# Performance work log

Hardware: AMD Instinct MI355X
Metric: run time of the kernel (lower is better)

## Reference

```python
import jax, jax.numpy as jnp
import numpy as np

D_MODEL = 1024
NHEAD = 16
D_HEAD = D_MODEL // NHEAD


def setup_inputs() -> dict:
    key = jax.random.key(0)
    ks = jax.random.split(key, 5)
    s_in = 1.0 / np.sqrt(D_MODEL)
    x = jax.random.normal(ks[0], (2, 2048, D_MODEL), dtype=jnp.float32)
    Wqkv = jax.random.uniform(ks[1], (D_MODEL, 3 * D_MODEL), jnp.float32, -s_in, s_in)
    bqkv = jax.random.uniform(ks[2], (3 * D_MODEL,), jnp.float32, -s_in, s_in)
    Wproj = jax.random.uniform(ks[3], (D_MODEL, D_MODEL), jnp.float32, -s_in, s_in)
    bproj = jax.random.uniform(ks[4], (D_MODEL,), jnp.float32, -s_in, s_in)
    return {"x": x, "Wqkv": Wqkv, "bqkv": bqkv, "Wproj": Wproj, "bproj": bproj}


def reference(x, Wqkv, bqkv, Wproj, bproj):
    B, N, D = x.shape
    qkv = x @ Wqkv + bqkv                       # [B, N, 3D]
    q, k, v = jnp.split(qkv, 3, axis=-1)
    # [B, N, D] -> [B, H, N, d]
    def to_heads(t):
        return t.reshape(B, N, NHEAD, D_HEAD).transpose(0, 2, 1, 3)
    q, k, v = to_heads(q), to_heads(k), to_heads(v)
    scale = 1.0 / np.sqrt(D_HEAD).astype(np.float32)
    attn = jnp.einsum('bhqd,bhkd->bhqk', q, k) * scale
    attn = jax.nn.softmax(attn, axis=-1)
    y = jnp.einsum('bhqk,bhkd->bhqd', attn, v)  # [B, H, N, d]
    y = y.transpose(0, 2, 1, 3).reshape(B, N, D)
    return y @ Wproj + bproj
```

## Files before the change

### kernel.cpp

```cpp
#include <hip/hip_runtime.h>
#include <hip/hip_bf16.h>
#include <stdint.h>

typedef __hip_bfloat16 bf16;
typedef __attribute__((ext_vector_type(8))) short short8;
typedef __attribute__((ext_vector_type(4))) float f32x4;

#define QSCALE 0.18033688011f

__device__ __forceinline__ float fast_exp2(float x) {
#if __has_builtin(__builtin_amdgcn_exp2f)
  return __builtin_amdgcn_exp2f(x);
#else
  return exp2f(x);
#endif
}

__device__ __forceinline__ uint32_t pack2_bf16(float a, float b) {
#if __has_builtin(__builtin_amdgcn_cvt_pk_bf16_f32)
  typedef __attribute__((ext_vector_type(2))) __bf16 bf16x2;
  bf16x2 v = __builtin_amdgcn_cvt_pk_bf16_f32(a, b);
  return __builtin_bit_cast(uint32_t, v);
#else
  uint32_t ua = __builtin_bit_cast(uint32_t, a);
  uint32_t ub = __builtin_bit_cast(uint32_t, b);
  ua += 0x7FFF + ((ua >> 16) & 1);
  ub += 0x7FFF + ((ub >> 16) & 1);
  return (ua >> 16) | (ub & 0xFFFF0000u);
#endif
}

__device__ __forceinline__ void gload_lds16(const bf16* g, bf16* l) {
#if __has_builtin(__builtin_amdgcn_global_load_lds)
  __builtin_amdgcn_global_load_lds(
      (const __attribute__((address_space(1))) void*)(uintptr_t)g,
      (__attribute__((address_space(3))) void*)(uint32_t)(uintptr_t)l,
      16, 0, 0);
#else
  int lane = threadIdx.x & 63;
  *(short8*)(l + lane * 8) = *(const short8*)(g + lane * 8);
#endif
}

#define VM4_BARRIER() \
  asm volatile("s_waitcnt vmcnt(4)\n\ts_barrier" ::: "memory")
#define VM3_BARRIER() \
  asm volatile("s_waitcnt vmcnt(3)\n\ts_barrier" ::: "memory")
#define LDSR_BARRIER() \
  asm volatile("s_waitcnt lgkmcnt(0)\n\ts_barrier" ::: "memory")
#define DMA_BARRIER() \
  asm volatile("s_waitcnt vmcnt(0) lgkmcnt(0)\n\ts_barrier" ::: "memory")

__device__ __forceinline__ void transpose_tile(const float* __restrict__ in,
                                               bf16* __restrict__ out,
                                               int R, int C, int bx, int by,
                                               bf16 (*t)[72]) {
  const int r0 = by * 64, c0 = bx * 64;
  const int rr = threadIdx.x >> 3, cc = (threadIdx.x & 7) * 8;
#pragma unroll
  for (int rep = 0; rep < 2; ++rep) {
    int y = rr + rep * 32;
    const float* p = in + (size_t)(r0 + y) * C + c0 + cc;
    f32x4 v0 = *(const f32x4*)p;
    f32x4 v1 = *(const f32x4*)(p + 4);
#pragma unroll
    for (int j = 0; j < 4; ++j) {
      t[cc + j][y] = __float2bfloat16(v0[j]);
      t[cc + 4 + j][y] = __float2bfloat16(v1[j]);
    }
  }
  __syncthreads();
#pragma unroll
  for (int rep = 0; rep < 2; ++rep) {
    int y = rr + rep * 32;
    short8 v = *(const short8*)&t[y][cc];
    *(short8*)(out + (size_t)(c0 + y) * R + r0 + cc) = v;
  }
}

__global__ __launch_bounds__(256)
void prep_k(const float* __restrict__ x, bf16* __restrict__ xb,
            const float* __restrict__ Wqkv, bf16* __restrict__ WtQkv,
            const float* __restrict__ Wproj, bf16* __restrict__ WtP) {
  __shared__ __align__(16) bf16 t[64][72];
  const int bid = blockIdx.x;
  if (bid < 2048) {
    int i = (bid * 256 + threadIdx.x) * 8;
    f32x4 v0 = *(const f32x4*)(x + i);
    f32x4 v1 = *(const f32x4*)(x + i + 4);
    short8 r;
    bf16* rb = (bf16*)&r;
#pragma unroll
    for (int j = 0; j < 4; ++j) {
      rb[j] = __float2bfloat16(v0[j]);
      rb[4 + j] = __float2bfloat16(v1[j]);
    }
    *(short8*)(xb + i) = r;
  } else if (bid < 2048 + 768) {
    int b = bid - 2048;
    transpose_tile(Wqkv, WtQkv, 1024, 3072, b % 48, b / 48, t);
  } else {
    int b = bid - 2816;
    transpose_tile(Wproj, WtP, 1024, 1024, b % 16, b / 16, t);
  }
}

template <int MODE, int TM>
__global__ __launch_bounds__(256, (TM == 128) ? 3 : 2)
void gemm_bt(const bf16* __restrict__ A, const bf16* __restrict__ Bt,
             const float* __restrict__ bias, float* __restrict__ outp,
             bf16* __restrict__ Qd, bf16* __restrict__ Kd, bf16* __restrict__ Vt,
             int M, int Nn, int K) {
  constexpr int MI = TM / 32;
  constexpr int BUFE = TM * 32 + 4096;
  __shared__ __align__(16) bf16 smem[2 * BUFE];

  const int tid = threadIdx.x;
  const int wave = tid >> 6, lane = tid & 63;
  const int quad = lane >> 4, l16 = lane & 15;
  const int mw = (wave >> 1) * (TM / 2), nw = (wave & 1) * 64;

  const int nwg = gridDim.x * gridDim.y;
  const int ord = blockIdx.y * gridDim.x + blockIdx.x;
  const int wg = (ord & 7) * (nwg >> 3) + (ord >> 3);
  const int m_blk = (wg / gridDim.x) * TM, n_blk = (wg % gridDim.x) * 128;

  f32x4 acc[MI][4];
#pragma unroll
  for (int i = 0; i < MI; ++i)
#pragma unroll
    for (int j = 0; j < 4; ++j) acc[i][j] = (f32x4){0.f, 0.f, 0.f, 0.f};

  const int rowA = lane >> 2, colA = (lane & 3) * 8;
  const int chunkB = wave * 2;
  const bf16* gB = Bt + (size_t)(n_blk + chunkB * 16 + rowA) * K + colA;
  const int chunkA = (TM == 128) ? wave * 2 : wave;
  const bf16* gA = A + (size_t)(m_blk + chunkA * 16 + rowA) * K + colA;

  const int oA0 = chunkA * 512;
  const int oA1 = (chunkA + 1) * 512;
  const int oB0 = TM * 32 + chunkB * 512;
  const int oB1 = TM * 32 + (chunkB + 1) * 512;

  gload_lds16(gA, smem + oA0);
  if (TM == 128) gload_lds16(gA + 16 * K, smem + oA1);
  gload_lds16(gB, smem + oB0);
  gload_lds16(gB + 16 * K, smem + oB1);

  for (int kt = 0; kt < K; kt += 32) {
    const int cur = (kt >> 5) & 1;
    bf16* bufc = smem + cur * BUFE;

    {
      const int kn = (kt + 32 < K) ? (kt + 32) : (K - 32);
      bf16* bufn = smem + (cur ^ 1) * BUFE;
      gload_lds16(gA + kn, bufn + oA0);
      if (TM == 128) gload_lds16(gA + 16 * K + kn, bufn + oA1);
      gload_lds16(gB + kn, bufn + oB0);
      gload_lds16(gB + 16 * K + kn, bufn + oB1);
    }

    if constexpr (TM == 128) VM4_BARRIER(); else VM3_BARRIER();

    short8 af[MI], bfv[4];
#pragma unroll
    for (int i = 0; i < MI; ++i)
      af[i] = *(const short8*)&bufc[(mw + i * 16 + l16) * 32 + quad * 8];
#pragma unroll
    for (int j = 0; j < 4; ++j)
      bfv[j] = *(const short8*)&bufc[TM * 32 + (nw + j * 16 + l16) * 32 + quad * 8];
#pragma unroll
    for (int i = 0; i < MI; ++i)
#pragma unroll
      for (int j = 0; j < 4; ++j)
        acc[i][j] = __builtin_amdgcn_mfma_f32_16x16x32_bf16(af[i], bfv[j],
                                                            acc[i][j], 0, 0, 0);

    LDSR_BARRIER();
  }

  DMA_BARRIER();

  if (MODE == 0) {
    float bval[4];
#pragma unroll
    for (int j = 0; j < 4; ++j) bval[j] = bias[n_blk + nw + j * 16 + l16];

    const int part = n_blk >> 10;
    const int b = m_blk >> 11;
    const int tloc = m_blk & 2047;
    const int h0 = (n_blk & 1023) >> 6;

#pragma unroll
    for (int p = 0; p < 2; ++p) {
      __syncthreads();
      if ((nw >> 6) == p) {
        if (part == 2) {
#pragma unroll
          for (int i = 0; i < MI; ++i)
#pragma unroll
            for (int j = 0; j < 4; ++j) {
              const int dh = j * 16 + l16;
              const int t0 = mw + i * 16 + quad * 4;
              uint2 pk;
              pk.x = pack2_bf16(acc[i][j][0] + bval[j], acc[i][j][1] + bval[j]);
              pk.y = pack2_bf16(acc[i][j][2] + bval[j], acc[i][j][3] + bval[j]);
              *(uint2*)&smem[dh * 136 + t0] = pk;
            }
        } else {
          const float sc = (part == 0) ? QSCALE : 1.0f;
#pragma unroll
          for (int i = 0; i < MI; ++i)
#pragma unroll
            for (int j = 0; j < 4; ++j) {
              const int d = j * 16 + l16;
              const int t0 = mw + i * 16 + quad * 4;
#pragma unroll
              for (int r = 0; r < 4; ++r)
                smem[(t0 + r) * 72 + d] =
                    __float2bfloat16((acc[i][j][r] + bval[j]) * sc);
            }
        }
      }
      __syncthreads();
      const size_t bh = (size_t)(b * 16 + h0 + p);
      if (part == 2) {
#pragma unroll
        for (int it = 0; it < 4; ++it) {
          const int dl = (tid >> 4) + it * 16;
          const int t8 = (tid & 15) * 8;
          const int t8s = (t8 & 64) | ((t8 ^ ((dl & 7) << 3)) & 63);
          short8 v = *(const short8*)&smem[dl * 136 + t8];
          *(short8*)&Vt[(bh * 64 + dl) * 2048 + tloc + t8s] = v;
        }
      } else {
        bf16* dst = (part == 0) ? Qd : Kd;
#pragma unroll
        for (int it = 0; it < 4; ++it) {
          const int row = (tid >> 3) + it * 32;
          const int col8 = (tid & 7) * 8;
          const int c8 = (part == 1) ? (col8 ^ ((row & 7) << 3)) : col8;
          short8 v = *(const short8*)&smem[row * 72 + col8];
          *(short8*)&dst[(bh * 2048 + tloc + row) * 64 + c8] = v;
        }
      }
    }
  } else {
#pragma unroll
    for (int j = 0; j < 4; ++j) {
      const int ncol = n_blk + nw + j * 16 + l16;
      const float bval = bias[ncol];
#pragma unroll
      for (int i = 0; i < MI; ++i) {
        const int mrow0 = m_blk + mw + i * 16 + quad * 4;
#pragma unroll
        for (int r = 0; r < 4; ++r)
          outp[(size_t)(mrow0 + r) * Nn + ncol] = acc[i][j][r] + bval;
      }
    }
  }
}

__global__ __launch_bounds__(256, 4)
void attn_kernel(const bf16* __restrict__ Qg, const bf16* __restrict__ Kg,
                 const bf16* __restrict__ Vt, bf16* __restrict__ yg) {
  __shared__ __align__(16) char pool[32768];
  bf16* KsB = (bf16*)pool;
  bf16* VtsB = (bf16*)(pool + 16384);

  const int tid = threadIdx.x;
  const int wave = tid >> 6, lane = tid & 63;
  const int quad = lane >> 4, l16 = lane & 15;
  const int qh = wave & 1, kvh = wave >> 1;

  const int bx0 = blockIdx.x;
  const int bx = ((bx0 & 7) << 7) | (bx0 >> 3);
  const int qt = bx & 31;
  const int bh = bx >> 5;

  const bf16* Qb = Qg + ((size_t)bh * 2048 + qt * 64) * 64;
  const bf16* Kb = Kg + (size_t)bh * 2048 * 64;
  const bf16* Vtb = Vt + (size_t)bh * 64 * 2048;

  short8 qf[2][2];
#pragma unroll
  for (int qblk = 0; qblk < 2; ++qblk)
#pragma unroll
    for (int ks = 0; ks < 2; ++ks)
      qf[qblk][ks] = *(const short8*)(
          Qb + (size_t)(qh * 32 + qblk * 16 + l16) * 64 + ks * 32 + quad * 8);

  const int sj = wave * 2;
  const bf16* kg = Kb + sj * 512 + lane * 8;
  const bf16* vg = Vtb + (size_t)(sj * 8 + (lane >> 3)) * 2048 +
                   (lane & 7) * 8;

  int kfo[2][2];
#pragma unroll
  for (int kvblk = 0; kvblk < 2; ++kvblk)
#pragma unroll
    for (int ks = 0; ks < 2; ++ks)
      kfo[kvblk][ks] = (kvh * 32 + kvblk * 16 + l16) * 64 +
                       (((ks * 4 + quad) ^ (l16 & 7)) << 3);
  int vbo[4][2];
#pragma unroll
  for (int dblk = 0; dblk < 4; ++dblk) {
    const int d = dblk * 16 + l16;
#pragma unroll
    for (int kvblk = 0; kvblk < 2; ++kvblk) {
      const int ct = kvh * 4 + kvblk * 2 + (quad >> 1);
      vbo[dblk][kvblk] = d * 64 + ((ct ^ (d & 7)) << 3) + (quad & 1) * 4;
    }
  }

#pragma unroll
  for (int j = 0; j < 2; ++j) {
    gload_lds16(kg + j * 512, KsB + sj * 512 + j * 512);
    gload_lds16(vg + (size_t)j * 16384, VtsB + sj * 512 + j * 512);
  }

  f32x4 yacc[2][4];
#pragma unroll
  for (int qblk = 0; qblk < 2; ++qblk)
#pragma unroll
    for (int dblk = 0; dblk < 4; ++dblk)
      yacc[qblk][dblk] = (f32x4){0.f, 0.f, 0.f, 0.f};
  f32x4 sum_acc[2];
  sum_acc[0] = (f32x4){0.f, 0.f, 0.f, 0.f};
  sum_acc[1] = (f32x4){0.f, 0.f, 0.f, 0.f};

  uint4 ones_u;
  ones_u.x = ones_u.y = ones_u.z = ones_u.w = 0x3F803F80u;
  const short8 ones8 = __builtin_bit_cast(short8, ones_u);

  for (int kt = 0; kt < 2048; kt += 64) {
    const int cur = (kt >> 6) & 1;

    {
      const int kn = (kt + 64 < 2048) ? (kt + 64) : (2048 - 64);
      bf16* Kdst = KsB + (cur ^ 1) * 4096;
      bf16* Vdst = VtsB + (cur ^ 1) * 4096;
#pragma unroll
      for (int j = 0; j < 2; ++j) {
        gload_lds16(kg + kn * 64 + j * 512, Kdst + sj * 512 + j * 512);
        gload_lds16(vg + kn + (size_t)j * 16384, Vdst + sj * 512 + j * 512);
      }
    }

    VM4_BARRIER();

    const bf16* KsC = KsB + cur * 4096;
    const bf16* VtsC = VtsB + cur * 4096;

    short8 kf[2][2];
#pragma unroll
    for (int kvblk = 0; kvblk < 2; ++kvblk)
#pragma unroll
      for (int ks = 0; ks < 2; ++ks)
        kf[kvblk][ks] = *(const short8*)(KsC + kfo[kvblk][ks]);

    short8 pa8[2];
#pragma unroll
    for (int qblk = 0; qblk < 2; ++qblk) {
      f32x4 s0 = (f32x4){0.f, 0.f, 0.f, 0.f};
      f32x4 s1 = (f32x4){0.f, 0.f, 0.f, 0.f};
      s0 = __builtin_amdgcn_mfma_f32_16x16x32_bf16(kf[0][0], qf[qblk][0], s0, 0, 0, 0);
      s0 = __builtin_amdgcn_mfma_f32_16x16x32_bf16(kf[0][1], qf[qblk][1], s0, 0, 0, 0);
      s1 = __builtin_amdgcn_mfma_f32_16x16x32_bf16(kf[1][0], qf[qblk][0], s1, 0, 0, 0);
      s1 = __builtin_amdgcn_mfma_f32_16x16x32_bf16(kf[1][1], qf[qblk][1], s1, 0, 0, 0);
      float p0 = fast_exp2(s0[0]), p1 = fast_exp2(s0[1]);
      float p2 = fast_exp2(s0[2]), p3 = fast_exp2(s0[3]);
      float p4 = fast_exp2(s1[0]), p5 = fast_exp2(s1[1]);
      float p6 = fast_exp2(s1[2]), p7 = fast_exp2(s1[3]);
      uint4 u;
      u.x = pack2_bf16(p0, p1);
      u.y = pack2_bf16(p2, p3);
      u.z = pack2_bf16(p4, p5);
      u.w = pack2_bf16(p6, p7);
      pa8[qblk] = __builtin_bit_cast(short8, u);
      sum_acc[qblk] = __builtin_amdgcn_mfma_f32_16x16x32_bf16(
          pa8[qblk], ones8, sum_acc[qblk], 0, 0, 0);
    }

#pragma unroll
    for (int dblk = 0; dblk < 4; ++dblk) {
      uint2 lo = *(const uint2*)(VtsC + vbo[dblk][0]);
      uint2 hi = *(const uint2*)(VtsC + vbo[dblk][1]);
      uint4 u;
      u.x = lo.x; u.y = lo.y; u.z = hi.x; u.w = hi.y;
      short8 vb8 = __builtin_bit_cast(short8, u);
      yacc[0][dblk] = __builtin_amdgcn_mfma_f32_16x16x32_bf16(
          pa8[0], vb8, yacc[0][dblk], 0, 0, 0);
      yacc[1][dblk] = __builtin_amdgcn_mfma_f32_16x16x32_bf16(
          pa8[1], vb8, yacc[1][dblk], 0, 0, 0);
    }

    LDSR_BARRIER();
  }

  DMA_BARRIER();
  float* red = (float*)pool;
  float* sred = (float*)(pool + 16384);
  if (kvh == 1) {
#pragma unroll
    for (int qblk = 0; qblk < 2; ++qblk) {
#pragma unroll
      for (int dblk = 0; dblk < 4; ++dblk) {
        const int f = (qh * 2 + qblk) * 4 + dblk;
        *(f32x4*)&red[(f * 64 + quad * 16 + l16) * 4] = yacc[qblk][dblk];
      }
      if (l16 == 0)
        *(f32x4*)&sred[(qh * 2 + qblk) * 16 + quad * 4] = sum_acc[qblk];
    }
  }
  __syncthreads();
  if (kvh == 0) {
    const int b = bh >> 4, h = bh & 15;
    const size_t rowbase = (size_t)b * 2048 + qt * 64;
#pragma unroll
    for (int qblk = 0; qblk < 2; ++qblk) {
      f32x4 sp = *(const f32x4*)&sred[(qh * 2 + qblk) * 16 + quad * 4];
#pragma unroll
      for (int dblk = 0; dblk < 4; ++dblk) {
        const int f = (qh * 2 + qblk) * 4 + dblk;
        f32x4 o = *(const f32x4*)&red[(f * 64 + quad * 16 + l16) * 4];
#pragma unroll
        for (int r = 0; r < 4; ++r) yacc[qblk][dblk][r] += o[r];
      }
#pragma unroll
      for (int r = 0; r < 4; ++r) {
        const float inv = 1.f / (sum_acc[qblk][r] + sp[r]);
        const int rr = qh * 32 + qblk * 16 + quad * 4 + r;
#pragma unroll
        for (int dblk = 0; dblk < 4; ++dblk)
          yg[(rowbase + rr) * 1024 + h * 64 + dblk * 16 + l16] =
              __float2bfloat16(yacc[qblk][dblk][r] * inv);
      }
    }
  }
}

extern "C" void kernel_launch(void* const* d_in, const int* in_sizes, int n_in,
                              void* d_out, int out_size, void* d_ws, size_t ws_size,
                              hipStream_t stream) {
  const float* x = (const float*)d_in[0];
  const float* Wqkv = (const float*)d_in[1];
  const float* bqkv = (const float*)d_in[2];
  const float* Wproj = (const float*)d_in[3];
  const float* bproj = (const float*)d_in[4];
  float* out = (float*)d_out;

  if (ws_size < (size_t)40 * 1024 * 1024) return;

  char* ws = (char*)d_ws;
  bf16* xb    = (bf16*)(ws + 0);
  bf16* yd    = (bf16*)(ws + 0);
  bf16* WtQkv = (bf16*)(ws + 8388608);
  bf16* WtP   = (bf16*)(ws + 14680064);
  bf16* Qd    = (bf16*)(ws + 16777216);
  bf16* Kd    = (bf16*)(ws + 25165824);
  bf16* Vten  = (bf16*)(ws + 33554432);

  prep_k<<<3072, 256, 0, stream>>>(x, xb, Wqkv, WtQkv, Wproj, WtP);
  gemm_bt<0, 128><<<dim3(24, 32), 256, 0, stream>>>(
      xb, WtQkv, bqkv, nullptr, Qd, Kd, Vten, 4096, 3072, 1024);
  attn_kernel<<<dim3(1024), 256, 0, stream>>>(Qd, Kd, Vten, yd);
  gemm_bt<1, 64><<<dim3(8, 64), 256, 0, stream>>>(
      yd, WtP, bproj, out, nullptr, nullptr, nullptr, 4096, 1024, 1024);
}
```

Measured before the change: 185.6 us.

## Triple-buffer GEMM K-loop and pre-permute V layout for single 16B LDS reads

After: 180.5 us. 2.7% less time.

```diff
diff --git a/kernel.cpp b/kernel.cpp
--- a/kernel.cpp
+++ b/kernel.cpp
@@ -113,7 +113,7 @@
              int M, int Nn, int K) {
   constexpr int MI = TM / 32;
   constexpr int BUFE = TM * 32 + 4096;
-  __shared__ __align__(16) bf16 smem[2 * BUFE];
+  __shared__ __align__(16) bf16 smem[3 * BUFE];
 
   const int tid = threadIdx.x;
   const int wave = tid >> 6, lane = tid & 63;
@@ -142,26 +142,25 @@
   const int oB0 = TM * 32 + chunkB * 512;
   const int oB1 = TM * 32 + (chunkB + 1) * 512;
 
-  gload_lds16(gA, smem + oA0);
-  if (TM == 128) gload_lds16(gA + 16 * K, smem + oA1);
-  gload_lds16(gB, smem + oB0);
-  gload_lds16(gB + 16 * K, smem + oB1);
-
-  for (int kt = 0; kt < K; kt += 32) {
-    const int cur = (kt >> 5) & 1;
-    bf16* bufc = smem + cur * BUFE;
-
-    {
-      const int kn = (kt + 32 < K) ? (kt + 32) : (K - 32);
-      bf16* bufn = smem + (cur ^ 1) * BUFE;
-      gload_lds16(gA + kn, bufn + oA0);
-      if (TM == 128) gload_lds16(gA + 16 * K + kn, bufn + oA1);
-      gload_lds16(gB + kn, bufn + oB0);
-      gload_lds16(gB + 16 * K + kn, bufn + oB1);
-    }
-
+  const int nI = K >> 5;
+  auto issue = [&](int t, int buf) {
+    bf16* b = smem + buf * BUFE;
+    const int kk = t << 5;
+    gload_lds16(gA + kk, b + oA0);
+    if (TM == 128) gload_lds16(gA + 16 * K + kk, b + oA1);
+    gload_lds16(gB + kk, b + oB0);
+    gload_lds16(gB + 16 * K + kk, b + oB1);
+  };
+
+  issue(0, 0);
+  issue(1, 1);
+
+  for (int it = 0; it < nI; ++it) {
     if constexpr (TM == 128) VM4_BARRIER(); else VM3_BARRIER();
 
+    issue((it + 2 < nI) ? it + 2 : nI - 1, (it + 2) % 3);
+
+    bf16* bufc = smem + (it % 3) * BUFE;
     short8 af[MI], bfv[4];
 #pragma unroll
     for (int i = 0; i < MI; ++i)
@@ -175,8 +174,6 @@
       for (int j = 0; j < 4; ++j)
         acc[i][j] = __builtin_amdgcn_mfma_f32_16x16x32_bf16(af[i], bfv[j],
                                                             acc[i][j], 0, 0, 0);
-
-    LDSR_BARRIER();
   }
 
   DMA_BARRIER();
@@ -229,9 +226,18 @@
         for (int it = 0; it < 4; ++it) {
           const int dl = (tid >> 4) + it * 16;
           const int t8 = (tid & 15) * 8;
-          const int t8s = (t8 & 64) | ((t8 ^ ((dl & 7) << 3)) & 63);
           short8 v = *(const short8*)&smem[dl * 136 + t8];
-          *(short8*)&Vt[(bh * 64 + dl) * 2048 + tloc + t8s] = v;
+          const int c = (t8 & 63) >> 3;
+          const int kvh = c >> 2, cc = c & 3;
+          const int q0 = (cc * 2) & 3, q1 = (cc * 2 + 1) & 3;
+          const int e2 = cc >> 1;
+          const int x7 = dl & 7;
+          const size_t rowb = (bh * 64 + dl) * 2048 + tloc + (t8 & 64);
+          uint4 u = __builtin_bit_cast(uint4, v);
+          *(uint2*)&Vt[rowb + (((kvh * 4 + q0) ^ x7) << 3) + e2 * 4] =
+              (uint2){u.x, u.y};
+          *(uint2*)&Vt[rowb + (((kvh * 4 + q1) ^ x7) << 3) + e2 * 4] =
+              (uint2){u.z, u.w};
         }
       } else {
         bf16* dst = (part == 0) ? Qd : Kd;
@@ -302,15 +308,11 @@
     for (int ks = 0; ks < 2; ++ks)
       kfo[kvblk][ks] = (kvh * 32 + kvblk * 16 + l16) * 64 +
                        (((ks * 4 + quad) ^ (l16 & 7)) << 3);
-  int vbo[4][2];
+  int vro[4];
 #pragma unroll
   for (int dblk = 0; dblk < 4; ++dblk) {
     const int d = dblk * 16 + l16;
-#pragma unroll
-    for (int kvblk = 0; kvblk < 2; ++kvblk) {
-      const int ct = kvh * 4 + kvblk * 2 + (quad >> 1);
-      vbo[dblk][kvblk] = d * 64 + ((ct ^ (d & 7)) << 3) + (quad & 1) * 4;
-    }
+    vro[dblk] = d * 64 + (((kvh * 4 + quad) ^ (d & 7)) << 3);
   }
 
 #pragma unroll
@@ -384,11 +386,7 @@
 
 #pragma unroll
     for (int dblk = 0; dblk < 4; ++dblk) {
-      uint2 lo = *(const uint2*)(VtsC + vbo[dblk][0]);
-      uint2 hi = *(const uint2*)(VtsC + vbo[dblk][1]);
-      uint4 u;
-      u.x = lo.x; u.y = lo.y; u.z = hi.x; u.w = hi.y;
-      short8 vb8 = __builtin_bit_cast(short8, u);
+      short8 vb8 = *(const short8*)(VtsC + vro[dblk]);
       yacc[0][dblk] = __builtin_amdgcn_mfma_f32_16x16x32_bf16(
           pa8[0], vb8, yacc[0][dblk], 0, 0, 0);
       yacc[1][dblk] = __builtin_amdgcn_mfma_f32_16x16x32_bf16(
```
